# Kernel tuning notes

Measured on AMD Instinct MI355X. Metric: run time of the kernel, lower is better.

Reference implementation:

```python
import jax, jax.numpy as jnp
import numpy as np

B, S, E, H = 4, 2048, 1024, 16
D = E // H  # head dim = 64


def setup_inputs() -> dict:
    key = jax.random.key(0)
    ks = jax.random.split(key, 8)
    scale = 0.02
    return {
        "query": jax.random.normal(ks[0], (B, S, E), jnp.float32),
        "keys": jax.random.normal(ks[1], (B, S, E), jnp.float32),
        "values": jax.random.normal(ks[2], (B, S, E), jnp.float32),
        "mask": jnp.ones((B, 1, 1, S), jnp.int32),
        "Wq": jax.random.normal(ks[3], (D, D), jnp.float32) * scale,
        "Wk": jax.random.normal(ks[4], (D, D), jnp.float32) * scale,
        "Wv": jax.random.normal(ks[5], (D, D), jnp.float32) * scale,
        "Wf": jax.random.normal(ks[6], (E, E), jnp.float32) * scale,
        "bf": jax.random.normal(ks[7], (E,), jnp.float32) * scale,
    }


def reference(query, keys, values, mask, Wq, Wk, Wv, Wf, bf):
    b, sq, _ = query.shape
    sk = keys.shape[1]
    # reshape to heads: [b, s, H, D]
    q = query.reshape(b, sq, H, D)
    k = keys.reshape(b, sk, H, D)
    v = values.reshape(b, sk, H, D)
    # per-head linear projections (torch Linear: x @ W.T, no bias)
    q = jnp.einsum('bshd,ed->bshe', q, Wq)
    k = jnp.einsum('bshd,ed->bshe', k, Wk)
    v = jnp.einsum('bshd,ed->bshe', v, Wv)
    # scores [b, h, q, k]
    scores = jnp.einsum('bqhd,bkhd->bhqk', q, k)
    scores = jnp.where(mask == 0, -jnp.inf, scores)
    attn = jax.nn.softmax(scores / jnp.sqrt(jnp.float32(D)), axis=3)
    # context [b, q, h, d] -> [b, q, E]
    ctx = jnp.einsum('bhqk,bkhd->bqhd', attn, v).reshape(b, sq, E)
    return ctx @ Wf.T + bf
```

## Files before the change

### kernel.cpp

```cpp
#include <hip/hip_runtime.h>

#define B_ 4
#define S_ 2048
#define E_ 1024
#define H_ 16
#define D_ 64

typedef unsigned short u16;
typedef unsigned int u32;
typedef __bf16 bf16x8 __attribute__((ext_vector_type(8)));
typedef float f32x4 __attribute__((ext_vector_type(4)));
typedef u16 u16x8 __attribute__((ext_vector_type(8)));
typedef u16 u16x4 __attribute__((ext_vector_type(4)));

#if defined(__has_builtin)
#if __has_builtin(__builtin_amdgcn_exp2f)
#define EXP2F(x) __builtin_amdgcn_exp2f(x)
#else
#define EXP2F(x) exp2f(x)
#endif
#else
#define EXP2F(x) exp2f(x)
#endif

__device__ __forceinline__ u16 bfbits(float f) {
  __bf16 h = (__bf16)f;
  return __builtin_bit_cast(u16, h);
}
__device__ __forceinline__ f32x4 mfma16(bf16x8 a, bf16x8 b, f32x4 c) {
  return __builtin_amdgcn_mfma_f32_16x16x32_bf16(a, b, c, 0, 0, 0);
}
__device__ __forceinline__ bf16x8 lds_ld8(const u16* base, int off) {
  return *reinterpret_cast<const bf16x8*>(reinterpret_cast<const char*>(base) + off);
}
__device__ __forceinline__ void gload_lds16(const u16* g, u16* l) {
  __builtin_amdgcn_global_load_lds((const __attribute__((address_space(1))) void*)g,
                                   (__attribute__((address_space(3))) void*)l, 16, 0, 0);
}

__global__ __launch_bounds__(256) void proj_kernel(
    const float* __restrict__ qin, const float* __restrict__ kin, const float* __restrict__ vin,
    const float* __restrict__ Wq, const float* __restrict__ Wk, const float* __restrict__ Wv,
    const float* __restrict__ Wf,
    u16* __restrict__ qo, u16* __restrict__ ko, u16* __restrict__ vo, u16* __restrict__ wfo)
{
  const int t = threadIdx.x;
  const int tensor = blockIdx.z >> 2, b = blockIdx.z & 3;

  if (tensor == 3) {
    int chunk = ((blockIdx.z & 3) * 16 + blockIdx.y) * 16 + blockIdx.x;
    int i = chunk * 256 + t;
    float4 f = reinterpret_cast<const float4*>(Wf)[i];
    u16x4 h4;
    h4[0] = bfbits(f.x); h4[1] = bfbits(f.y); h4[2] = bfbits(f.z); h4[3] = bfbits(f.w);
    reinterpret_cast<u16x4*>(wfo)[i] = h4;
    return;
  }

  __shared__ __align__(16) u16 Al[128 * 64];
  __shared__ __align__(16) u16 Wl[64 * 64];
  const int w = t >> 6, l = t & 63, lg = l >> 4, ln = l & 15;
  const int h = blockIdx.y, s0 = blockIdx.x * 128;

  const float* x; const float* W; float scale;
  if (tensor == 0)      { x = qin; W = Wq; scale = 0.125f * 1.44269504f; }
  else if (tensor == 1) { x = kin; W = Wk; scale = 1.0f; }
  else                  { x = vin; W = Wv; scale = 1.0f; }

  {
    const int e = t >> 2, d0 = (t & 3) * 16;
    const float4* wr = reinterpret_cast<const float4*>(W + e * 64 + d0);
    float4 f0 = wr[0], f1 = wr[1], f2 = wr[2], f3 = wr[3];
    u16x8 p0, p1;
    p0[0]=bfbits(f0.x*scale); p0[1]=bfbits(f0.y*scale); p0[2]=bfbits(f0.z*scale); p0[3]=bfbits(f0.w*scale);
    p0[4]=bfbits(f1.x*scale); p0[5]=bfbits(f1.y*scale); p0[6]=bfbits(f1.z*scale); p0[7]=bfbits(f1.w*scale);
    p1[0]=bfbits(f2.x*scale); p1[1]=bfbits(f2.y*scale); p1[2]=bfbits(f2.z*scale); p1[3]=bfbits(f2.w*scale);
    p1[4]=bfbits(f3.x*scale); p1[5]=bfbits(f3.y*scale); p1[6]=bfbits(f3.z*scale); p1[7]=bfbits(f3.w*scale);
    *reinterpret_cast<u16x8*>(reinterpret_cast<char*>(Wl) + ((e*128 + d0*2     ) ^ ((e & 7) << 4))) = p0;
    *reinterpret_cast<u16x8*>(reinterpret_cast<char*>(Wl) + ((e*128 + d0*2 + 16) ^ ((e & 7) << 4))) = p1;
  }
  {
    const int row = t >> 1, d0 = (t & 1) * 32;
    const float4* xr = reinterpret_cast<const float4*>(x + ((size_t)(b * S_ + s0 + row)) * E_ + h * D_ + d0);
    #pragma unroll
    for (int c = 0; c < 4; ++c) {
      float4 f0 = xr[2 * c], f1 = xr[2 * c + 1];
      u16x8 pk;
      pk[0]=bfbits(f0.x); pk[1]=bfbits(f0.y); pk[2]=bfbits(f0.z); pk[3]=bfbits(f0.w);
      pk[4]=bfbits(f1.x); pk[5]=bfbits(f1.y); pk[6]=bfbits(f1.z); pk[7]=bfbits(f1.w);
      *reinterpret_cast<u16x8*>(reinterpret_cast<char*>(Al) +
          ((row * 128 + (d0 + 8 * c) * 2) ^ ((row & 7) << 4))) = pk;
    }
  }
  __syncthreads();

  bf16x8 wb[4][2];
  #pragma unroll
  for (int nn = 0; nn < 4; ++nn) {
    int brow = nn * 16 + ln;
    int bo = (brow * 128 + lg * 16) ^ ((ln & 7) << 4);
    wb[nn][0] = lds_ld8(Wl, bo);
    wb[nn][1] = lds_ld8(Wl, bo ^ 64);
  }
  f32x4 acc[2][4] = {};
  #pragma unroll
  for (int sub = 0; sub < 2; ++sub) {
    int arow = 32 * w + 16 * sub + ln;
    int ao = (arow * 128 + lg * 16) ^ ((ln & 7) << 4);
    bf16x8 a0 = lds_ld8(Al, ao), a1 = lds_ld8(Al, ao ^ 64);
    #pragma unroll
    for (int nn = 0; nn < 4; ++nn) {
      acc[sub][nn] = mfma16(a0, wb[nn][0], acc[sub][nn]);
      acc[sub][nn] = mfma16(a1, wb[nn][1], acc[sub][nn]);
    }
  }

  if (tensor < 2) {
    u16* o = (tensor == 0) ? qo : ko;
    const size_t hb = ((size_t)(b * H_ + h)) * (S_ * D_);
    #pragma unroll
    for (int sub = 0; sub < 2; ++sub)
      #pragma unroll
      for (int nn = 0; nn < 4; ++nn)
        #pragma unroll
        for (int r = 0; r < 4; ++r)
          o[hb + (size_t)(s0 + 32*w + 16*sub + 4*lg + r) * D_ + nn*16 + ln] = bfbits(acc[sub][nn][r]);
  } else {
    const size_t hb = ((size_t)(b * H_ + h)) * (D_ * S_);
    #pragma unroll
    for (int sub = 0; sub < 2; ++sub)
      #pragma unroll
      for (int nn = 0; nn < 4; ++nn)
        #pragma unroll
        for (int r = 0; r < 4; ++r) {
          int scol = s0 + 32*w + 16*sub + 4*lg + r;
          int sl = scol & 63;
          int c = (sl & 3) | (((sl >> 4) & 1) << 2) | (((sl >> 2) & 3) << 3) | ((sl >> 5) << 5);
          vo[hb + (size_t)(nn*16 + ln) * S_ + (scol & ~63) + c] = bfbits(acc[sub][nn][r]);
        }
  }
}

__global__ __launch_bounds__(256, 2) void attn_kernel(
    const u16* __restrict__ qw,
    const u16* __restrict__ kw,
    const u16* __restrict__ vtw,
    const int* __restrict__ mask,
    u16* __restrict__ ctx)
{
  __shared__ __align__(16) u16 Kl[2][64 * 64];
  __shared__ __align__(16) u16 Vl[2][64 * 64];
  __shared__ int s_allone;

  const int t = threadIdx.x, w = t >> 6, l = t & 63, lg = l >> 4, ln = l & 15;
  const int hb = blockIdx.x;
  const int b = hb >> 4;
  const int q0 = blockIdx.y * 256;
  const size_t koff = (size_t)hb * (S_ * D_);
  const size_t voff = (size_t)hb * (D_ * S_);

  if (t == 0) s_allone = 1;
  __syncthreads();

  const int srow = t >> 3, scol = (t & 7) ^ ((t >> 3) & 7);
  const u16* kg = kw + koff + srow * D_ + scol * 8;
  const u16* vg = vtw + voff + (size_t)srow * S_ + scol * 8;
  u16* kd = &Kl[0][0] + t * 8;
  u16* vd = &Vl[0][0] + t * 8;

  gload_lds16(kg, kd);
  gload_lds16(kg + 32 * D_, kd + 2048);
  gload_lds16(vg, vd);
  gload_lds16(vg + (size_t)32 * S_, vd + 2048);

  {
    const int4 m0 = *reinterpret_cast<const int4*>(mask + b * S_ + t * 8);
    const int4 m1 = *reinterpret_cast<const int4*>(mask + b * S_ + t * 8 + 4);
    if (!(m0.x && m0.y && m0.z && m0.w && m1.x && m1.y && m1.z && m1.w)) s_allone = 0;
  }

  bf16x8 qb[4][2];
  #pragma unroll
  for (int sub = 0; sub < 4; ++sub) {
    const u16* qp = qw + koff + (size_t)(q0 + 64*w + 16*sub + ln) * D_ + 8*lg;
    qb[sub][0] = *reinterpret_cast<const bf16x8*>(qp);
    qb[sub][1] = *reinterpret_cast<const bf16x8*>(qp + 32);
  }

  u16x8 ob;
  #pragma unroll
  for (int i = 0; i < 8; ++i) ob[i] = 0x3F80;
  const bf16x8 ones = __builtin_bit_cast(bf16x8, ob);

  f32x4 oacc[4][4] = {};
  f32x4 lacc[4] = {};

  asm volatile("s_waitcnt vmcnt(0)" ::: "memory");
  __syncthreads();
  const int allone = s_allone;

  int cur = 0;
  for (int kt = 0; kt < S_ / 64; ++kt) {
    if (kt + 1 < S_ / 64) {
      const int nk = (kt + 1) * 64;
      u16* kdn = kd + (cur ^ 1) * 4096;
      u16* vdn = vd + (cur ^ 1) * 4096;
      gload_lds16(kg + nk * D_, kdn);
      gload_lds16(kg + (nk + 32) * D_, kdn + 2048);
      gload_lds16(vg + nk, vdn);
      gload_lds16(vg + (size_t)32 * S_ + nk, vdn + 2048);
    }
    const u16* Kc = &Kl[cur][0];
    const u16* Vc = &Vl[cur][0];

    bf16x8 pa[4][2];
    #pragma unroll
    for (int sp = 0; sp < 2; ++sp) {
      f32x4 sc[2][4];
      __builtin_amdgcn_s_setprio(1);
      #pragma unroll
      for (int kn = 0; kn < 4; ++kn) {
        int o0 = ((ln * 128 + lg * 16) ^ ((ln & 7) << 4)) + kn * 2048;
        bf16x8 ka0 = lds_ld8(Kc, o0), ka1 = lds_ld8(Kc, o0 ^ 64);
        #pragma unroll
        for (int s2 = 0; s2 < 2; ++s2) {
          f32x4 z = {0.f, 0.f, 0.f, 0.f};
          z = mfma16(ka0, qb[sp * 2 + s2][0], z);
          z = mfma16(ka1, qb[sp * 2 + s2][1], z);
          sc[s2][kn] = z;
        }
      }
      __builtin_amdgcn_s_setprio(0);

      if (!allone) {
        const int kv0 = kt * 64;
        #pragma unroll
        for (int kn = 0; kn < 4; ++kn) {
          const int4 m4 = *reinterpret_cast<const int4*>(mask + b * S_ + kv0 + kn * 16 + lg * 4);
          const int* mp = reinterpret_cast<const int*>(&m4);
          #pragma unroll
          for (int r = 0; r < 4; ++r)
            if (mp[r] == 0) { sc[0][kn][r] = -1e30f; sc[1][kn][r] = -1e30f; }
        }
      }

      #pragma unroll
      for (int s2 = 0; s2 < 2; ++s2)
        #pragma unroll
        for (int kn = 0; kn < 4; ++kn)
          #pragma unroll
          for (int r = 0; r < 4; ++r)
            pa[sp * 2 + s2][kn >> 1][(kn & 1) * 4 + r] = (__bf16)EXP2F(sc[s2][kn][r]);
    }

    __builtin_amdgcn_s_setprio(1);
    #pragma unroll
    for (int sub = 0; sub < 4; ++sub) {
      lacc[sub] = mfma16(pa[sub][0], ones, lacc[sub]);
      lacc[sub] = mfma16(pa[sub][1], ones, lacc[sub]);
    }
    #pragma unroll
    for (int kh = 0; kh < 2; ++kh) {
      #pragma unroll
      for (int dn = 0; dn < 4; ++dn) {
        int vo0 = ((ln * 128 + 16 * lg + 64 * kh) ^ ((ln & 7) << 4)) + dn * 2048;
        bf16x8 vb = lds_ld8(Vc, vo0);
        #pragma unroll
        for (int sub = 0; sub < 4; ++sub)
          oacc[sub][dn] = mfma16(pa[sub][kh], vb, oacc[sub][dn]);
      }
    }
    __builtin_amdgcn_s_setprio(0);

    if (kt + 1 < S_ / 64) {
      asm volatile("s_waitcnt vmcnt(0)" ::: "memory");
      __syncthreads();
      cur ^= 1;
    }
  }

  #pragma unroll
  for (int sub = 0; sub < 4; ++sub) {
    #pragma unroll
    for (int r = 0; r < 4; ++r) {
      float linv = 1.f / lacc[sub][r];
      int qrow = q0 + 64 * w + 16 * sub + 4 * lg + r;
      size_t base = ((size_t)b * S_ + qrow) * E_ + (hb & 15) * D_;
      #pragma unroll
      for (int dn = 0; dn < 4; ++dn)
        ctx[base + dn * 16 + ln] = bfbits(oacc[sub][dn][r] * linv);
    }
  }
}

__global__ __launch_bounds__(256, 2) void outproj_kernel(
    const u16* __restrict__ ctx, const u16* __restrict__ wf,
    const float* __restrict__ bias, float* __restrict__ out)
{
  __shared__ __align__(16) u16 Al[2][128 * 64];
  __shared__ __align__(16) u16 Bl[2][128 * 64];
  const int t = threadIdx.x, w = t >> 6, l = t & 63, lg = l >> 4, ln = l & 15;
  const int wm = w >> 1, wn = w & 1;
  const int m0 = blockIdx.x * 128, n0 = blockIdx.y * 128;
  f32x4 acc[4][4] = {};

  const u16* ag[4]; const u16* bg[4]; int ldo[4];
  #pragma unroll
  for (int it = 0; it < 4; ++it) {
    int j = it * 256 + t, row = j >> 3, c = (j & 7) ^ (row & 7);
    ag[it] = ctx + (size_t)(m0 + row) * E_ + c * 8;
    bg[it] = wf  + (size_t)(n0 + row) * E_ + c * 8;
    ldo[it] = j * 8;
  }
  #pragma unroll
  for (int it = 0; it < 4; ++it) {
    gload_lds16(ag[it], &Al[0][0] + ldo[it]);
    gload_lds16(bg[it], &Bl[0][0] + ldo[it]);
  }
  asm volatile("s_waitcnt vmcnt(0)" ::: "memory");
  __syncthreads();

  int cur = 0;
  for (int kt = 0; kt < E_ / 64; ++kt) {
    if (kt + 1 < E_ / 64) {
      const int k0 = (kt + 1) * 64;
      #pragma unroll
      for (int it = 0; it < 4; ++it) {
        gload_lds16(ag[it] + k0, &Al[cur ^ 1][0] + ldo[it]);
        gload_lds16(bg[it] + k0, &Bl[cur ^ 1][0] + ldo[it]);
      }
    }
    const u16* Ac = &Al[cur][0]; const u16* Bc = &Bl[cur][0];

    bf16x8 af[4][2], bff[4][2];
    #pragma unroll
    for (int ms = 0; ms < 4; ++ms) {
      int ar = 64 * wm + 16 * ms + ln;
      int ao = (ar * 128 + lg * 16) ^ ((ln & 7) << 4);
      af[ms][0] = lds_ld8(Ac, ao); af[ms][1] = lds_ld8(Ac, ao ^ 64);
    }
    #pragma unroll
    for (int ns = 0; ns < 4; ++ns) {
      int br = 64 * wn + 16 * ns + ln;
      int bo = (br * 128 + lg * 16) ^ ((ln & 7) << 4);
      bff[ns][0] = lds_ld8(Bc, bo); bff[ns][1] = lds_ld8(Bc, bo ^ 64);
    }
    __builtin_amdgcn_s_setprio(1);
    #pragma unroll
    for (int ms = 0; ms < 4; ++ms)
      #pragma unroll
      for (int ns = 0; ns < 4; ++ns) {
        acc[ms][ns] = mfma16(af[ms][0], bff[ns][0], acc[ms][ns]);
        acc[ms][ns] = mfma16(af[ms][1], bff[ns][1], acc[ms][ns]);
      }
    __builtin_amdgcn_s_setprio(0);

    if (kt + 1 < E_ / 64) {
      asm volatile("s_waitcnt vmcnt(0)" ::: "memory");
      __syncthreads();
      cur ^= 1;
    }
  }

  #pragma unroll
  for (int ns = 0; ns < 4; ++ns) {
    float bv = bias[n0 + 64 * wn + 16 * ns + ln];
    #pragma unroll
    for (int ms = 0; ms < 4; ++ms)
      #pragma unroll
      for (int r = 0; r < 4; ++r)
        out[(size_t)(m0 + 64*wm + 16*ms + 4*lg + r) * E_ + n0 + 64*wn + 16*ns + ln] =
            acc[ms][ns][r] + bv;
  }
}

extern "C" void kernel_launch(void* const* d_in, const int* in_sizes, int n_in,
                              void* d_out, int out_size, void* d_ws, size_t ws_size,
                              hipStream_t stream)
{
  const float* q   = (const float*)d_in[0];
  const float* k   = (const float*)d_in[1];
  const float* v   = (const float*)d_in[2];
  const int*  mask = (const int*) d_in[3];
  const float* Wq  = (const float*)d_in[4];
  const float* Wk  = (const float*)d_in[5];
  const float* Wv  = (const float*)d_in[6];
  const float* Wf  = (const float*)d_in[7];
  const float* bfv = (const float*)d_in[8];
  float* out = (float*)d_out;

  const size_t NQKV = (size_t)B_ * H_ * S_ * D_;
  const size_t NCTX = (size_t)B_ * S_ * E_;
  u16* q_ws   = (u16*)d_ws;
  u16* k_ws   = q_ws + NQKV;
  u16* v_ws   = k_ws + NQKV;
  u16* ctx_ws = v_ws + NQKV;
  u16* wf_ws  = ctx_ws + NCTX;

  proj_kernel<<<dim3(S_ / 128, H_, 16), dim3(256), 0, stream>>>(
      q, k, v, Wq, Wk, Wv, Wf, q_ws, k_ws, v_ws, wf_ws);
  attn_kernel<<<dim3(B_ * H_, S_ / 256), dim3(256), 0, stream>>>(
      q_ws, k_ws, v_ws, mask, ctx_ws);
  outproj_kernel<<<dim3((B_ * S_) / 128, E_ / 128), dim3(256), 0, stream>>>(
      ctx_ws, wf_ws, bfv, out);
}
```

Baseline: 118.8 us.

## Use 512-thread attention blocks with 32 query rows per wave

The attention kernel now runs 8 waves per block instead of 4. Each wave covers 32 query rows instead of 64, and each thread stages one K and one V chunk per tile instead of two. This raises occupancy and latency hiding and lowers per-wave register pressure. In exchange, each LDS-loaded K/V fragment is reused by fewer MFMAs, so LDS read traffic per FLOP rises, and barriers now synchronize more waves.

```diff
diff --git a/kernel.cpp b/kernel.cpp
--- a/kernel.cpp
+++ b/kernel.cpp
@@ -141,7 +141,7 @@
   }
 }
 
-__global__ __launch_bounds__(256, 2) void attn_kernel(
+__global__ __launch_bounds__(512, 4) void attn_kernel(
     const u16* __restrict__ qw,
     const u16* __restrict__ kw,
     const u16* __restrict__ vtw,
@@ -169,20 +169,17 @@
   u16* vd = &Vl[0][0] + t * 8;
 
   gload_lds16(kg, kd);
-  gload_lds16(kg + 32 * D_, kd + 2048);
   gload_lds16(vg, vd);
-  gload_lds16(vg + (size_t)32 * S_, vd + 2048);
 
   {
-    const int4 m0 = *reinterpret_cast<const int4*>(mask + b * S_ + t * 8);
-    const int4 m1 = *reinterpret_cast<const int4*>(mask + b * S_ + t * 8 + 4);
-    if (!(m0.x && m0.y && m0.z && m0.w && m1.x && m1.y && m1.z && m1.w)) s_allone = 0;
-  }
-
-  bf16x8 qb[4][2];
-  #pragma unroll
-  for (int sub = 0; sub < 4; ++sub) {
-    const u16* qp = qw + koff + (size_t)(q0 + 64*w + 16*sub + ln) * D_ + 8*lg;
+    const int4 m4 = *reinterpret_cast<const int4*>(mask + b * S_ + t * 4);
+    if (!(m4.x && m4.y && m4.z && m4.w)) s_allone = 0;
+  }
+
+  bf16x8 qb[2][2];
+  #pragma unroll
+  for (int sub = 0; sub < 2; ++sub) {
+    const u16* qp = qw + koff + (size_t)(q0 + 32*w + 16*sub + ln) * D_ + 8*lg;
     qb[sub][0] = *reinterpret_cast<const bf16x8*>(qp);
     qb[sub][1] = *reinterpret_cast<const bf16x8*>(qp + 32);
   }
@@ -192,8 +189,8 @@
   for (int i = 0; i < 8; ++i) ob[i] = 0x3F80;
   const bf16x8 ones = __builtin_bit_cast(bf16x8, ob);
 
-  f32x4 oacc[4][4] = {};
-  f32x4 lacc[4] = {};
+  f32x4 oacc[2][4] = {};
+  f32x4 lacc[2] = {};
 
   asm volatile("s_waitcnt vmcnt(0)" ::: "memory");
   __syncthreads();
@@ -203,73 +200,65 @@
   for (int kt = 0; kt < S_ / 64; ++kt) {
     if (kt + 1 < S_ / 64) {
       const int nk = (kt + 1) * 64;
-      u16* kdn = kd + (cur ^ 1) * 4096;
-      u16* vdn = vd + (cur ^ 1) * 4096;
-      gload_lds16(kg + nk * D_, kdn);
-      gload_lds16(kg + (nk + 32) * D_, kdn + 2048);
-      gload_lds16(vg + nk, vdn);
-      gload_lds16(vg + (size_t)32 * S_ + nk, vdn + 2048);
+      gload_lds16(kg + nk * D_, kd + (cur ^ 1) * 4096);
+      gload_lds16(vg + nk,      vd + (cur ^ 1) * 4096);
     }
     const u16* Kc = &Kl[cur][0];
     const u16* Vc = &Vl[cur][0];
 
-    bf16x8 pa[4][2];
-    #pragma unroll
-    for (int sp = 0; sp < 2; ++sp) {
-      f32x4 sc[2][4];
-      __builtin_amdgcn_s_setprio(1);
+    f32x4 sc[2][4];
+    __builtin_amdgcn_s_setprio(1);
+    #pragma unroll
+    for (int kn = 0; kn < 4; ++kn) {
+      int o0 = ((ln * 128 + lg * 16) ^ ((ln & 7) << 4)) + kn * 2048;
+      bf16x8 ka0 = lds_ld8(Kc, o0), ka1 = lds_ld8(Kc, o0 ^ 64);
+      #pragma unroll
+      for (int sub = 0; sub < 2; ++sub) {
+        f32x4 z = {0.f, 0.f, 0.f, 0.f};
+        z = mfma16(ka0, qb[sub][0], z);
+        z = mfma16(ka1, qb[sub][1], z);
+        sc[sub][kn] = z;
+      }
+    }
+    __builtin_amdgcn_s_setprio(0);
+
+    if (!allone) {
+      const int kv0 = kt * 64;
       #pragma unroll
       for (int kn = 0; kn < 4; ++kn) {
-        int o0 = ((ln * 128 + lg * 16) ^ ((ln & 7) << 4)) + kn * 2048;
-        bf16x8 ka0 = lds_ld8(Kc, o0), ka1 = lds_ld8(Kc, o0 ^ 64);
-        #pragma unroll
-        for (int s2 = 0; s2 < 2; ++s2) {
-          f32x4 z = {0.f, 0.f, 0.f, 0.f};
-          z = mfma16(ka0, qb[sp * 2 + s2][0], z);
-          z = mfma16(ka1, qb[sp * 2 + s2][1], z);
-          sc[s2][kn] = z;
-        }
-      }
-      __builtin_amdgcn_s_setprio(0);
-
-      if (!allone) {
-        const int kv0 = kt * 64;
-        #pragma unroll
-        for (int kn = 0; kn < 4; ++kn) {
-          const int4 m4 = *reinterpret_cast<const int4*>(mask + b * S_ + kv0 + kn * 16 + lg * 4);
-          const int* mp = reinterpret_cast<const int*>(&m4);
-          #pragma unroll
-          for (int r = 0; r < 4; ++r)
-            if (mp[r] == 0) { sc[0][kn][r] = -1e30f; sc[1][kn][r] = -1e30f; }
-        }
-      }
-
-      #pragma unroll
-      for (int s2 = 0; s2 < 2; ++s2)
-        #pragma unroll
-        for (int kn = 0; kn < 4; ++kn)
-          #pragma unroll
-          for (int r = 0; r < 4; ++r)
-            pa[sp * 2 + s2][kn >> 1][(kn & 1) * 4 + r] = (__bf16)EXP2F(sc[s2][kn][r]);
-    }
+        const int4 m4 = *reinterpret_cast<const int4*>(mask + b * S_ + kv0 + kn * 16 + lg * 4);
+        const int* mp = reinterpret_cast<const int*>(&m4);
+        #pragma unroll
+        for (int r = 0; r < 4; ++r)
+          if (mp[r] == 0) { sc[0][kn][r] = -1e30f; sc[1][kn][r] = -1e30f; }
+      }
+    }
+
+    bf16x8 pa[2][2];
+    #pragma unroll
+    for (int sub = 0; sub < 2; ++sub)
+      #pragma unroll
+      for (int kn = 0; kn < 4; ++kn)
+        #pragma unroll
+        for (int r = 0; r < 4; ++r)
+          pa[sub][kn >> 1][(kn & 1) * 4 + r] = (__bf16)EXP2F(sc[sub][kn][r]);
 
     __builtin_amdgcn_s_setprio(1);
     #pragma unroll
-    for (int sub = 0; sub < 4; ++sub) {
+    for (int sub = 0; sub < 2; ++sub) {
       lacc[sub] = mfma16(pa[sub][0], ones, lacc[sub]);
       lacc[sub] = mfma16(pa[sub][1], ones, lacc[sub]);
     }
     #pragma unroll
-    for (int kh = 0; kh < 2; ++kh) {
+    for (int kh = 0; kh < 2; ++kh)
       #pragma unroll
       for (int dn = 0; dn < 4; ++dn) {
         int vo0 = ((ln * 128 + 16 * lg + 64 * kh) ^ ((ln & 7) << 4)) + dn * 2048;
         bf16x8 vb = lds_ld8(Vc, vo0);
         #pragma unroll
-        for (int sub = 0; sub < 4; ++sub)
+        for (int sub = 0; sub < 2; ++sub)
           oacc[sub][dn] = mfma16(pa[sub][kh], vb, oacc[sub][dn]);
       }
-    }
     __builtin_amdgcn_s_setprio(0);
 
     if (kt + 1 < S_ / 64) {
@@ -280,11 +269,11 @@
   }
 
   #pragma unroll
-  for (int sub = 0; sub < 4; ++sub) {
+  for (int sub = 0; sub < 2; ++sub) {
     #pragma unroll
     for (int r = 0; r < 4; ++r) {
       float linv = 1.f / lacc[sub][r];
-      int qrow = q0 + 64 * w + 16 * sub + 4 * lg + r;
+      int qrow = q0 + 32 * w + 16 * sub + 4 * lg + r;
       size_t base = ((size_t)b * S_ + qrow) * E_ + (hb & 15) * D_;
       #pragma unroll
       for (int dn = 0; dn < 4; ++dn)
@@ -399,7 +388,7 @@
 
   proj_kernel<<<dim3(S_ / 128, H_, 16), dim3(256), 0, stream>>>(
       q, k, v, Wq, Wk, Wv, Wf, q_ws, k_ws, v_ws, wf_ws);
-  attn_kernel<<<dim3(B_ * H_, S_ / 256), dim3(256), 0, stream>>>(
+  attn_kernel<<<dim3(B_ * H_, S_ / 256), dim3(512), 0, stream>>>(
       q_ws, k_ws, v_ws, mask, ctx_ws);
   outproj_kernel<<<dim3((B_ * S_) / 128, E_ / 128), dim3(256), 0, stream>>>(
       ctx_ws, wf_ws, bfv, out);
```

After: 120.5 us. About the same (+1.4%).
